# Performance work log

Hardware: AMD Instinct MI355X
Metric: run time of the kernel (lower is better)

The kernel has to match this reference:

```python
import jax, jax.numpy as jnp
import numpy as np

N, E, D, H, C, G, L = 50000, 1250000, 128, 64, 10, 128, 2


def setup_inputs() -> dict:
    key = jax.random.key(0)
    ks = jax.random.split(key, 18)
    s = lambda fan_in: 1.0 / np.sqrt(fan_in)
    inp = {
        "x": jax.random.normal(ks[0], (N, D), dtype=jnp.float32),
        "edge_index": jax.random.randint(ks[1], (2, E), 0, N, dtype=jnp.int64),
        "batch": jnp.sort(jax.random.randint(ks[2], (N,), 0, G, dtype=jnp.int64)),
        # node embedding MLP (D->H->H)
        "emb_w1": jax.random.uniform(ks[3], (D, H), jnp.float32, -s(D), s(D)),
        "emb_b1": jnp.zeros((H,), jnp.float32),
        "emb_w2": jax.random.uniform(ks[4], (H, H), jnp.float32, -s(H), s(H)),
        "emb_b2": jnp.zeros((H,), jnp.float32),
        # per-conv-block params, stacked over L layers
        "rel_w": jax.random.uniform(ks[5], (L, H, H), jnp.float32, -s(H), s(H)),
        "rel_b": jnp.zeros((L, H), jnp.float32),
        "root_w": jax.random.uniform(ks[6], (L, H, H), jnp.float32, -s(H), s(H)),
        "post_w1": jax.random.uniform(ks[7], (L, H, H), jnp.float32, -s(H), s(H)),
        "post_b1": jnp.zeros((L, H), jnp.float32),
        "post_w2": jax.random.uniform(ks[8], (L, H, H), jnp.float32, -s(H), s(H)),
        "post_b2": jnp.zeros((L, H), jnp.float32),
        # classifier
        "cls_w": jax.random.uniform(ks[9], (H, C), jnp.float32, -s(H), s(H)),
        "cls_b": jnp.zeros((C,), jnp.float32),
    }
    return inp


def _mlp(h, w1, b1, w2, b2):
    # Linear -> relu -> (dropout: identity in eval) -> Linear
    return jax.nn.relu(h @ w1 + b1) @ w2 + b2


def reference(x, edge_index, batch, emb_w1, emb_b1, emb_w2, emb_b2,
              rel_w, rel_b, root_w, post_w1, post_b1, post_w2, post_b2,
              cls_w, cls_b):
    src, dst = edge_index[0], edge_index[1]
    h = _mlp(x, emb_w1, emb_b1, emb_w2, emb_b2)  # [N,H]
    deg = jax.ops.segment_sum(jnp.ones((E,), h.dtype), dst, num_segments=N)
    inv_deg = 1.0 / jnp.maximum(deg, 1.0)  # mean aggregation, isolated nodes -> 0
    for l in range(L):
        agg = jax.ops.segment_sum(h[src], dst, num_segments=N) * inv_deg[:, None]
        h = agg @ rel_w[l] + rel_b[l] + h @ root_w[l]  # GraphConv (lin_root bias-free)
        h = _mlp(h, post_w1[l], post_b1[l], post_w2[l], post_b2[l])
        h = jax.nn.relu(h)  # dropout is identity in eval
    cnt = jax.ops.segment_sum(jnp.ones((N,), h.dtype), batch, num_segments=G)
    pooled = jax.ops.segment_sum(h, batch, num_segments=G) / jnp.maximum(cnt, 1.0)[:, None]
    return pooled @ cls_w + cls_b  # [G,C]
```

## Files before the change

kernel.cpp:

```cpp
#include <hip/hip_runtime.h>

typedef unsigned int u32;
typedef unsigned short u16;

#define NN 50000
#define EE 1250000
#define DD 128
#define HH 64
#define NCLS 10
#define NG 128
#define MAXDEG 80

#define NTILES ((NN + 63) / 64)

#define PBUK 392
#define SBLK 256
#define CHUNK ((EE + SBLK - 1) / SBLK)
#define NDP  (PBUK * 128)
#define EPKB ((CHUNK * 4 + 15) & ~15)

#define WT_LO  (8 * 4096)
#define WT_E1  (16 * 4096)
#define WT_E1L (WT_E1 + 8192)
#define WT_E2  (WT_E1 + 16384)
#define WT_E2L (WT_E2 + 4096)
#define WT_TOT (WT_E2 + 8192)


__device__ __forceinline__ u32 f2bf(float f) {
    u32 u = __float_as_uint(f);
    return (u + 0x7FFFu + ((u >> 16) & 1u)) >> 16;
}
__device__ __forceinline__ float bf2f(u16 v) {
    return __uint_as_float(((u32)v) << 16);
}

typedef __attribute__((ext_vector_type(8))) short bf16x8;
typedef __attribute__((ext_vector_type(4))) float f32x4;


__global__ __launch_bounds__(256) void k_wprep(
    const float* __restrict__ rel_w, const float* __restrict__ root_w,
    const float* __restrict__ pw1, const float* __restrict__ pw2,
    const float* __restrict__ ew1, const float* __restrict__ ew2,
    u16* __restrict__ wtb) {
    __shared__ float ldsf[128 * 65];
    const int t = threadIdx.x;
    const int m = blockIdx.x;
    if (m < 8) {
        const int layer = m >> 2, which = m & 3;
        const float* srcw =
            (which == 0 ? rel_w : which == 1 ? root_w : which == 2 ? pw1 : pw2)
            + (size_t)layer * HH * HH;
        #pragma unroll
        for (int r = 0; r < 16; ++r) {
            int idx = r * 256 + t;
            int k = idx >> 6, n = idx & 63;
            ldsf[k * 65 + n] = srcw[idx];
        }
        __syncthreads();
        #pragma unroll
        for (int r = 0; r < 16; ++r) {
            int idx = r * 256 + t;
            int n = idx >> 6, k = idx & 63;
            float v = ldsf[k * 65 + n];
            u16 hi = (u16)f2bf(v);
            u16 lo = (u16)f2bf(v - bf2f(hi));
            wtb[m * 4096 + idx] = hi;
            wtb[WT_LO + m * 4096 + idx] = lo;
        }
    } else if (m == 8) {
        #pragma unroll
        for (int r = 0; r < 32; ++r) {
            int idx = r * 256 + t;
            int k = idx >> 6, n = idx & 63;
            ldsf[k * 65 + n] = ew1[idx];
        }
        __syncthreads();
        #pragma unroll
        for (int r = 0; r < 32; ++r) {
            int idx = r * 256 + t;
            int n = idx >> 7, k = idx & 127;
            float v = ldsf[k * 65 + n];
            u16 hi = (u16)f2bf(v);
            u16 lo = (u16)f2bf(v - bf2f(hi));
            wtb[WT_E1 + idx] = hi;
            wtb[WT_E1L + idx] = lo;
        }
    } else {
        #pragma unroll
        for (int r = 0; r < 16; ++r) {
            int idx = r * 256 + t;
            int k = idx >> 6, n = idx & 63;
            ldsf[k * 65 + n] = ew2[idx];
        }
        __syncthreads();
        #pragma unroll
        for (int r = 0; r < 16; ++r) {
            int idx = r * 256 + t;
            int n = idx >> 6, k = idx & 63;
            float v = ldsf[k * 65 + n];
            u16 hi = (u16)f2bf(v);
            u16 lo = (u16)f2bf(v - bf2f(hi));
            wtb[WT_E2 + idx] = hi;
            wtb[WT_E2L + idx] = lo;
        }
    }
}


__global__ __launch_bounds__(256) void k_embed_psort(
    const float* __restrict__ x,
    const float* __restrict__ b1, const float* __restrict__ b2,
    const u16* __restrict__ wtb,
    u16* __restrict__ hb,
    const int* __restrict__ ei, u32* __restrict__ bedges,
    int* __restrict__ gboff, int* __restrict__ ghist) {
    __shared__ __align__(16) char smem[EPKB + PBUK * 8 + 32];
    const int t = threadIdx.x;

    if (blockIdx.x < SBLK) {
        u32* epk   = (u32*)smem;
        int* hist  = (int*)(smem + EPKB);
        int* boffS = hist + PBUK;
        int* wsum  = boffS + PBUK;
        const int cb = blockIdx.x;
        const int base = cb * CHUNK;
        const int n = min(CHUNK, EE - base);

        for (int b = t; b < PBUK; b += 256) hist[b] = 0;
        __syncthreads();
        for (int i0 = t; i0 < n; i0 += 2048) {
            int sV[8], dV[8];
            #pragma unroll
            for (int j = 0; j < 8; ++j) {
                int i = i0 + j * 256;
                sV[j] = -1; dV[j] = -1;
                if (i < n) { sV[j] = ei[base + i]; dV[j] = ei[EE + base + i]; }
            }
            #pragma unroll
            for (int j = 0; j < 8; ++j) {
                int i = i0 + j * 256;
                if (i < n) {
                    bool ok = (unsigned)sV[j] < NN && (unsigned)dV[j] < NN;
                    u32 w = ok ? (((u32)(dV[j] >> 7) << 23) | ((u32)sV[j] << 7) | (u32)(dV[j] & 127))
                               : 0xFFFFFFFFu;
                    epk[i] = w;
                    if (ok) atomicAdd(&hist[dV[j] >> 7], 1);
                }
            }
        }
        __syncthreads();
        int v = 0, h0 = 0;
        if (t < PBUK / 2) { h0 = hist[2 * t]; v = h0 + hist[2 * t + 1]; }
        int lane = t & 63, wd = t >> 6;
        int incl = v;
        #pragma unroll
        for (int d = 1; d < 64; d <<= 1) {
            int tt = __shfl_up(incl, d);
            if (lane >= d) incl += tt;
        }
        if (lane == 63) wsum[wd] = incl;
        __syncthreads();
        int woff = 0;
        for (int w = 0; w < wd; ++w) woff += wsum[w];
        if (t < PBUK / 2) {
            int excl = woff + incl - v;
            boffS[2 * t] = excl;
// ... 57 lines not shown
            for (int tt = 0; tt < 4; ++tt) {
                const u16* ph = wtb + WT_E1 + (tt * 16 + lr) * 128 + kc * 32 + lg * 8;
                const u16* pl = wtb + WT_E1L + (tt * 16 + lr) * 128 + kc * 32 + lg * 8;
                bf16x8 wh = *(const bf16x8*)ph;
                bf16x8 wl = *(const bf16x8*)pl;
                acc[tt] = __builtin_amdgcn_mfma_f32_16x16x32_bf16(xh, wh, acc[tt], 0, 0, 0);
                acc[tt] = __builtin_amdgcn_mfma_f32_16x16x32_bf16(xl, wh, acc[tt], 0, 0, 0);
                acc[tt] = __builtin_amdgcn_mfma_f32_16x16x32_bf16(xh, wl, acc[tt], 0, 0, 0);
            }
        }
        #pragma unroll
        for (int tt = 0; tt < 4; ++tt)
            #pragma unroll
            for (int r = 0; r < 4; ++r) {
                float v = fmaxf(acc[tt][r], 0.0f);
                u16 hi = (u16)f2bf(v);
                u16 lo = (u16)f2bf(v - bf2f(hi));
                acts0[(rowb + lg * 4 + r) * 72 + tt * 16 + lr] = hi;
                acts1[(rowb + lg * 4 + r) * 72 + tt * 16 + lr] = lo;
            }
        __syncthreads();

        bf16x8 c0h = *(const bf16x8*)&acts0[(rowb + lr) * 72 + lg * 8];
        bf16x8 c1h = *(const bf16x8*)&acts0[(rowb + lr) * 72 + 32 + lg * 8];
        bf16x8 c0l = *(const bf16x8*)&acts1[(rowb + lr) * 72 + lg * 8];
        bf16x8 c1l = *(const bf16x8*)&acts1[(rowb + lr) * 72 + 32 + lg * 8];
        f32x4 acc2[4];
        #pragma unroll
        for (int tt = 0; tt < 4; ++tt) {
            float b = b2[tt * 16 + lr];
            acc2[tt] = (f32x4){b, b, b, b};
        }
        #pragma unroll
        for (int tt = 0; tt < 4; ++tt) {
            const u16* ph = wtb + WT_E2 + (tt * 16 + lr) * 64 + lg * 8;
            const u16* pl = wtb + WT_E2L + (tt * 16 + lr) * 64 + lg * 8;
            bf16x8 wh0 = *(const bf16x8*)ph;
            bf16x8 wh1 = *(const bf16x8*)(ph + 32);
            bf16x8 wl0 = *(const bf16x8*)pl;
            bf16x8 wl1 = *(const bf16x8*)(pl + 32);
            acc2[tt] = __builtin_amdgcn_mfma_f32_16x16x32_bf16(c0h, wh0, acc2[tt], 0, 0, 0);
            acc2[tt] = __builtin_amdgcn_mfma_f32_16x16x32_bf16(c1h, wh1, acc2[tt], 0, 0, 0);
            acc2[tt] = __builtin_amdgcn_mfma_f32_16x16x32_bf16(c0l, wh0, acc2[tt], 0, 0, 0);
            acc2[tt] = __builtin_amdgcn_mfma_f32_16x16x32_bf16(c1l, wh1, acc2[tt], 0, 0, 0);
            acc2[tt] = __builtin_amdgcn_mfma_f32_16x16x32_bf16(c0h, wl0, acc2[tt], 0, 0, 0);
            acc2[tt] = __builtin_amdgcn_mfma_f32_16x16x32_bf16(c1h, wl1, acc2[tt], 0, 0, 0);
        }
        #pragma unroll
        for (int tt = 0; tt < 4; ++tt)
            #pragma unroll
            for (int r = 0; r < 4; ++r) {
                int node = nb + rowb + lg * 4 + r;
                if (node < NN)
                    hb[(size_t)node * HH + tt * 16 + lr] = (u16)f2bf(acc2[tt][r]);
            }
    }
}


__global__ __launch_bounds__(256) void k_adj(const u32* __restrict__ bedges,
                                             const int* __restrict__ gboff,
                                             const int* __restrict__ ghist,
                                             u16* __restrict__ slots,
                                             int* __restrict__ deg,
                                             float* __restrict__ pooled,
                                             u16* __restrict__ hb) {
    __shared__ u16 ls[128 * MAXDEG];
    __shared__ int lc[128];
    const int b = blockIdx.x, t = threadIdx.x;
    const int lane = t & 63, wid = t >> 6;
    if (b < (NG * HH) / 256) pooled[b * 256 + t] = 0.0f;
    if (b == 0 && t < 32) ((u32*)hb)[NN * (HH / 2) + t] = 0;
    if (t < 128) lc[t] = 0;
    {
        const u32 sent = ((u32)NN << 16) | (u32)NN;
        u32* lsu = (u32*)ls;
        for (int i = t; i < 128 * MAXDEG / 2; i += 256) lsu[i] = sent;
    }
    const int sbl = wid * 64 + lane;
    const int offv = gboff[sbl * PBUK + b];
    const int cntv = ghist[sbl * PBUK + b];
    __syncthreads();
    const int q = lane >> 4, sl = lane & 15;
    for (int it = 0; it < 16; ++it) {
        const int idx = it * 4 + q;
        const int off = __shfl(offv, idx);
        const int cnt = __shfl(cntv, idx);
        const int gbase = (wid * 64 + idx) * CHUNK + off;
        for (int i = sl; i < cnt; i += 16) {
            u32 p = bedges[gbase + i];
            int o = (int)(p & 127u);
            int src = (int)(p >> 7);
            int pos = atomicAdd(&lc[o], 1);
            if (pos < MAXDEG) ls[o * MAXDEG + pos] = (u16)src;
        }
    }
    __syncthreads();
    u32* gs = (u32*)(slots + (size_t)b * 128 * MAXDEG);
    const u32* lsu = (const u32*)ls;
    for (int i = t; i < 128 * MAXDEG / 2; i += 256) gs[i] = lsu[i];
    if (t < 128) deg[b * 128 + t] = lc[t];
}


__global__ __launch_bounds__(256) void k_agg(
    const u16* __restrict__ hb, const int* __restrict__ deg,
    const u16* __restrict__ slots, u16* __restrict__ aggb) {
    const int wid = threadIdx.x >> 6, lane = threadIdx.x & 63;
    const int half = lane >> 5, fl = lane & 31;
    const int n0 = blockIdx.x * 8 + wid * 2;
    if (n0 >= NN) return;
    const int n = n0 + half;
    const bool valid = n < NN;
    const int d = valid ? deg[n] : 0;
    const int m = min(d, MAXDEG);
    const int mp = (m + 15) & ~15;
    const u32* row = (const u32*)(slots + (size_t)n * MAXDEG);
    float s0 = 0.0f, s1 = 0.0f;
    for (int e = 0; e < mp; e += 16) {
        const u32* rp = row + (e >> 1);
        uint4 i0 = *(const uint4*)rp;
        uint4 i1 = *(const uint4*)(rp + 4);
        u32 v0 = *(const u32*)(hb + (size_t)(i0.x & 0xffffu) * HH + 2 * fl);
        u32 v1 = *(const u32*)(hb + (size_t)(i0.x >> 16)    * HH + 2 * fl);
        u32 v2 = *(const u32*)(hb + (size_t)(i0.y & 0xffffu) * HH + 2 * fl);
        u32 v3 = *(const u32*)(hb + (size_t)(i0.y >> 16)    * HH + 2 * fl);
        u32 v4 = *(const u32*)(hb + (size_t)(i0.z & 0xffffu) * HH + 2 * fl);
        u32 v5 = *(const u32*)(hb + (size_t)(i0.z >> 16)    * HH + 2 * fl);
        u32 v6 = *(const u32*)(hb + (size_t)(i0.w & 0xffffu) * HH + 2 * fl);
        u32 v7 = *(const u32*)(hb + (size_t)(i0.w >> 16)    * HH + 2 * fl);
        u32 v8 = *(const u32*)(hb + (size_t)(i1.x & 0xffffu) * HH + 2 * fl);
        u32 v9 = *(const u32*)(hb + (size_t)(i1.x >> 16)    * HH + 2 * fl);
        u32 va = *(const u32*)(hb + (size_t)(i1.y & 0xffffu) * HH + 2 * fl);
        u32 vb = *(const u32*)(hb + (size_t)(i1.y >> 16)    * HH + 2 * fl);
        u32 vc = *(const u32*)(hb + (size_t)(i1.z & 0xffffu) * HH + 2 * fl);
        u32 vd = *(const u32*)(hb + (size_t)(i1.z >> 16)    * HH + 2 * fl);
        u32 ve = *(const u32*)(hb + (size_t)(i1.w & 0xffffu) * HH + 2 * fl);
        u32 vf = *(const u32*)(hb + (size_t)(i1.w >> 16)    * HH + 2 * fl);
        s0 += ((bf2f((u16)(v0 & 0xffffu)) + bf2f((u16)(v1 & 0xffffu)))
             + (bf2f((u16)(v2 & 0xffffu)) + bf2f((u16)(v3 & 0xffffu))))
            + ((bf2f((u16)(v4 & 0xffffu)) + bf2f((u16)(v5 & 0xffffu)))
             + (bf2f((u16)(v6 & 0xffffu)) + bf2f((u16)(v7 & 0xffffu))));
        s0 += ((bf2f((u16)(v8 & 0xffffu)) + bf2f((u16)(v9 & 0xffffu)))
             + (bf2f((u16)(va & 0xffffu)) + bf2f((u16)(vb & 0xffffu))))
            + ((bf2f((u16)(vc & 0xffffu)) + bf2f((u16)(vd & 0xffffu)))
             + (bf2f((u16)(ve & 0xffffu)) + bf2f((u16)(vf & 0xffffu))));
        s1 += ((bf2f((u16)(v0 >> 16)) + bf2f((u16)(v1 >> 16)))
             + (bf2f((u16)(v2 >> 16)) + bf2f((u16)(v3 >> 16))))
            + ((bf2f((u16)(v4 >> 16)) + bf2f((u16)(v5 >> 16)))
             + (bf2f((u16)(v6 >> 16)) + bf2f((u16)(v7 >> 16))));
        s1 += ((bf2f((u16)(v8 >> 16)) + bf2f((u16)(v9 >> 16)))
             + (bf2f((u16)(va >> 16)) + bf2f((u16)(vb >> 16))))
            + ((bf2f((u16)(vc >> 16)) + bf2f((u16)(vd >> 16)))
             + (bf2f((u16)(ve >> 16)) + bf2f((u16)(vf >> 16))));
    }
    if (valid) {
        float inv = 1.0f / (float)max(d, 1);
        u32 p = f2bf(s0 * inv) | (f2bf(s1 * inv) << 16);
        ((u32*)aggb)[(size_t)n * (HH / 2) + fl] = p;
    }
}


__global__ __launch_bounds__(256) void k_dense(
    u16* __restrict__ hb, const u16* __restrict__ aggb,
    const u16* __restrict__ wt,
    const float* __restrict__ relb,
    const float* __restrict__ pb1, const float* __restrict__ pb2,
    const int* __restrict__ batch, float* __restrict__ pooled, int do_pool) {
    __shared__ __align__(16) u16 acts[2][64][72];
    const int t = threadIdx.x;
    const int w = t >> 6;
    const int l = t & 63;
    const int lr = l & 15, lg = l >> 4;
    const int rowb = w * 16;
    const int nb = blockIdx.x * 64;
    int nodeA = nb + rowb + lr;
    if (nodeA >= NN) nodeA = NN - 1;

    const u16* w_rel = wt;
    const u16* w_root = wt + 4096;
    const u16* w_p1  = wt + 2 * 4096;
    const u16* w_p2  = wt + 3 * 4096;

    const u16* agp = aggb + (size_t)nodeA * HH + lg * 8;
    const u16* hbp = hb   + (size_t)nodeA * HH + lg * 8;
    bf16x8 a0 = *(const bf16x8*)agp;
    bf16x8 a1 = *(const bf16x8*)(agp + 32);
    bf16x8 h0 = *(const bf16x8*)hbp;
    bf16x8 h1 = *(const bf16x8*)(hbp + 32);

    f32x4 acc[4];
    #pragma unroll
    for (int tt = 0; tt < 4; ++tt) {
        float b = relb[tt * 16 + lr];
        acc[tt] = (f32x4){b, b, b, b};
    }
    #pragma unroll
    for (int tt = 0; tt < 4; ++tt) {
        const u16* pr = w_rel  + (tt * 16 + lr) * 64 + lg * 8;
        const u16* po = w_root + (tt * 16 + lr) * 64 + lg * 8;
        acc[tt] = __builtin_amdgcn_mfma_f32_16x16x32_bf16(a0, *(const bf16x8*)pr,                acc[tt], 0, 0, 0);
        acc[tt] = __builtin_amdgcn_mfma_f32_16x16x32_bf16(a1, *(const bf16x8*)(pr + 32),         acc[tt], 0, 0, 0);
        acc[tt] = __builtin_amdgcn_mfma_f32_16x16x32_bf16(a0, *(const bf16x8*)(pr + WT_LO),      acc[tt], 0, 0, 0);
        acc[tt] = __builtin_amdgcn_mfma_f32_16x16x32_bf16(a1, *(const bf16x8*)(pr + WT_LO + 32), acc[tt], 0, 0, 0);
        acc[tt] = __builtin_amdgcn_mfma_f32_16x16x32_bf16(h0, *(const bf16x8*)po,                acc[tt], 0, 0, 0);
        acc[tt] = __builtin_amdgcn_mfma_f32_16x16x32_bf16(h1, *(const bf16x8*)(po + 32),         acc[tt], 0, 0, 0);
        acc[tt] = __builtin_amdgcn_mfma_f32_16x16x32_bf16(h0, *(const bf16x8*)(po + WT_LO),      acc[tt], 0, 0, 0);
        acc[tt] = __builtin_amdgcn_mfma_f32_16x16x32_bf16(h1, *(const bf16x8*)(po + WT_LO + 32), acc[tt], 0, 0, 0);
    }
    #pragma unroll
    for (int tt = 0; tt < 4; ++tt)
        #pragma unroll
        for (int r = 0; r < 4; ++r)
            acts[0][rowb + lg * 4 + r][tt * 16 + lr] = (u16)f2bf(acc[tt][r]);
    __syncthreads();

    bf16x8 c0 = *(const bf16x8*)&acts[0][rowb + lr][lg * 8];
    bf16x8 c1 = *(const bf16x8*)&acts[0][rowb + lr][32 + lg * 8];
    f32x4 acc2[4];
    #pragma unroll
    for (int tt = 0; tt < 4; ++tt) {
        float b = pb1[tt * 16 + lr];
        acc2[tt] = (f32x4){b, b, b, b};
    }
    #pragma unroll
    for (int tt = 0; tt < 4; ++tt) {
        const u16* pr = w_p1 + (tt * 16 + lr) * 64 + lg * 8;
        acc2[tt] = __builtin_amdgcn_mfma_f32_16x16x32_bf16(c0, *(const bf16x8*)pr,                acc2[tt], 0, 0, 0);
        acc2[tt] = __builtin_amdgcn_mfma_f32_16x16x32_bf16(c1, *(const bf16x8*)(pr + 32),         acc2[tt], 0, 0, 0);
        acc2[tt] = __builtin_amdgcn_mfma_f32_16x16x32_bf16(c0, *(const bf16x8*)(pr + WT_LO),      acc2[tt], 0, 0, 0);
        acc2[tt] = __builtin_amdgcn_mfma_f32_16x16x32_bf16(c1, *(const bf16x8*)(pr + WT_LO + 32), acc2[tt], 0, 0, 0);
    }
    #pragma unroll
    for (int tt = 0; tt < 4; ++tt)
        #pragma unroll
        for (int r = 0; r < 4; ++r)
            acts[1][rowb + lg * 4 + r][tt * 16 + lr] = (u16)f2bf(fmaxf(acc2[tt][r], 0.0f));
    __syncthreads();

    bf16x8 d0 = *(const bf16x8*)&acts[1][rowb + lr][lg * 8];
    bf16x8 d1 = *(const bf16x8*)&acts[1][rowb + lr][32 + lg * 8];
    f32x4 acc3[4];
    #pragma unroll
    for (int tt = 0; tt < 4; ++tt) {
        float b = pb2[tt * 16 + lr];
        acc3[tt] = (f32x4){b, b, b, b};
    }
    #pragma unroll
    for (int tt = 0; tt < 4; ++tt) {
        const u16* pr = w_p2 + (tt * 16 + lr) * 64 + lg * 8;
        acc3[tt] = __builtin_amdgcn_mfma_f32_16x16x32_bf16(d0, *(const bf16x8*)pr,                acc3[tt], 0, 0, 0);
        acc3[tt] = __builtin_amdgcn_mfma_f32_16x16x32_bf16(d1, *(const bf16x8*)(pr + 32),         acc3[tt], 0, 0, 0);
        acc3[tt] = __builtin_amdgcn_mfma_f32_16x16x32_bf16(d0, *(const bf16x8*)(pr + WT_LO),      acc3[tt], 0, 0, 0);
        acc3[tt] = __builtin_amdgcn_mfma_f32_16x16x32_bf16(d1, *(const bf16x8*)(pr + WT_LO + 32), acc3[tt], 0, 0, 0);
    }

    if (!do_pool) {
        #pragma unroll
        for (int tt = 0; tt < 4; ++tt)
            #pragma unroll
            for (int r = 0; r < 4; ++r) {
                int node = nb + rowb + lg * 4 + r;
                if (node < NN)
                    hb[(size_t)node * HH + tt * 16 + lr] = (u16)f2bf(fmaxf(acc3[tt][r], 0.0f));
            }
    } else {
        #pragma unroll
        for (int tt = 0; tt < 4; ++tt)
            #pragma unroll
            for (int r = 0; r < 4; ++r)
                acts[0][rowb + lg * 4 + r][tt * 16 + lr] = (u16)f2bf(fmaxf(acc3[tt][r], 0.0f));
        __syncthreads();
        if (t < HH) {
            const int f = t;
            const int n1 = min(64, NN - nb);
            int cur = batch[nb];
            float s = 0.0f;
            for (int i = 0; i < n1; ++i) {
                int g = batch[nb + i];
                if (g != cur) {
                    if ((unsigned)cur < NG) atomicAdd(&pooled[cur * HH + f], s);
                    s = 0.0f; cur = g;
                }
                s += bf2f(acts[0][i][f]);
            }
            if ((unsigned)cur < NG) atomicAdd(&pooled[cur * HH + f], s);
        }
    }
}


__global__ void k_cls(const float* __restrict__ pooled, const int* __restrict__ batch,
                      const float* __restrict__ w, const float* __restrict__ b,
                      float* __restrict__ out) {
    const int g = blockIdx.x;
    const int t = threadIdx.x;
    if (t >= NCLS) return;
    int lo = 0, hi = NN;
    while (lo < hi) { int mid = (lo + hi) >> 1; if (batch[mid] < g) lo = mid + 1; else hi = mid; }
    const int beg = lo;
    lo = 0; hi = NN;
    while (lo < hi) { int mid = (lo + hi) >> 1; if (batch[mid] < g + 1) lo = mid + 1; else hi = mid; }
    const int cnt = lo - beg;
    const float inv = 1.0f / (float)max(cnt, 1);
    float o = b[t];
    #pragma unroll 8
    for (int k = 0; k < HH; ++k) o += pooled[g * HH + k] * inv * w[k * NCLS + t];
    out[g * NCLS + t] = o;
}


extern "C" void kernel_launch(void* const* d_in, const int* in_sizes, int n_in,
                              void* d_out, int out_size, void* d_ws, size_t ws_size,
                              hipStream_t stream) {
    const float* x      = (const float*)d_in[0];
    const int*   ei     = (const int*)d_in[1];
    const int*   batch  = (const int*)d_in[2];
    const float* emb_w1 = (const float*)d_in[3];
    const float* emb_b1 = (const float*)d_in[4];
    const float* emb_w2 = (const float*)d_in[5];
    const float* emb_b2 = (const float*)d_in[6];
    const float* rel_w  = (const float*)d_in[7];
    const float* rel_b  = (const float*)d_in[8];
    const float* root_w = (const float*)d_in[9];
    const float* pw1    = (const float*)d_in[10];
    const float* pb1    = (const float*)d_in[11];
    const float* pw2    = (const float*)d_in[12];
    const float* pb2    = (const float*)d_in[13];
    const float* cls_w  = (const float*)d_in[14];
    const float* cls_b  = (const float*)d_in[15];
    float* out = (float*)d_out;

    char* ws = (char*)d_ws;
    size_t off = 0;
    auto alloc = [&](size_t bytes) -> void* {
        off = (off + 255) & ~(size_t)255;
        void* p = ws + off;
        off += bytes;
        return p;
    };
    u16*   hb     = (u16*)alloc((size_t)(NN + 1) * HH * 2);
    u16*   aggb   = (u16*)alloc((size_t)NN * HH * 2);
    u32*   bedges = (u32*)aggb;
    u16*   slots  = (u16*)alloc((size_t)NDP * MAXDEG * 2);
    int*   deg    = (int*)alloc((size_t)NDP * 4);
    int*   gboff  = (int*)alloc((size_t)SBLK * PBUK * 4);
    int*   ghist  = (int*)alloc((size_t)SBLK * PBUK * 4);
    float* pooled = (float*)alloc((size_t)NG * HH * 4);
    u16*   wtb    = (u16*)alloc((size_t)WT_TOT * 2);

    k_wprep<<<10, 256, 0, stream>>>(rel_w, root_w, pw1, pw2, emb_w1, emb_w2, wtb);
    k_embed_psort<<<SBLK + NTILES, 256, 0, stream>>>(
        x, emb_b1, emb_b2, wtb, hb, ei, bedges, gboff, ghist);
    k_adj<<<PBUK, 256, 0, stream>>>(bedges, gboff, ghist, slots, deg, pooled, hb);
    k_agg<<<(NN + 7) / 8, 256, 0, stream>>>(hb, deg, slots, aggb);
    k_dense<<<NTILES, 256, 0, stream>>>(hb, aggb, wtb, rel_b, pb1, pb2, batch, pooled, 0);
    k_agg<<<(NN + 7) / 8, 256, 0, stream>>>(hb, deg, slots, aggb);
    k_dense<<<NTILES, 256, 0, stream>>>(hb, aggb, wtb + 4 * 4096,
                                        rel_b + HH, pb1 + HH, pb2 + HH,
                                        batch, pooled, 1);
    k_cls<<<NG, 64, 0, stream>>>(pooled, batch, cls_w, cls_b, out);
}
```

Before: 262.0 us.

## Fuse neighbor aggregation into dense kernel and fold classifier into last block

```diff
diff --git a/kernel.cpp b/kernel.cpp
--- a/kernel.cpp
+++ b/kernel.cpp
@@ -289,13 +289,19 @@
                                              u16* __restrict__ slots,
                                              int* __restrict__ deg,
                                              float* __restrict__ pooled,
-                                             u16* __restrict__ hb) {
+                                             u16* __restrict__ hbA,
+                                             u16* __restrict__ hbB,
+                                             int* __restrict__ ctr) {
     __shared__ u16 ls[128 * MAXDEG];
     __shared__ int lc[128];
     const int b = blockIdx.x, t = threadIdx.x;
     const int lane = t & 63, wid = t >> 6;
     if (b < (NG * HH) / 256) pooled[b * 256 + t] = 0.0f;
-    if (b == 0 && t < 32) ((u32*)hb)[NN * (HH / 2) + t] = 0;
+    if (b == 0) {
+        if (t < 32) ((u32*)hbA)[NN * (HH / 2) + t] = 0;
+        else if (t < 64) ((u32*)hbB)[NN * (HH / 2) + (t - 32)] = 0;
+        else if (t == 64) *ctr = 0;
+    }
     if (t < 128) lc[t] = 0;
     {
         const u32 sent = ((u32)NN << 16) | (u32)NN;
@@ -328,90 +334,94 @@
 }
 
 
-__global__ __launch_bounds__(256) void k_agg(
-    const u16* __restrict__ hb, const int* __restrict__ deg,
-    const u16* __restrict__ slots, u16* __restrict__ aggb) {
-    const int wid = threadIdx.x >> 6, lane = threadIdx.x & 63;
-    const int half = lane >> 5, fl = lane & 31;
-    const int n0 = blockIdx.x * 8 + wid * 2;
-    if (n0 >= NN) return;
-    const int n = n0 + half;
-    const bool valid = n < NN;
-    const int d = valid ? deg[n] : 0;
-    const int m = min(d, MAXDEG);
-    const int mp = (m + 15) & ~15;
-    const u32* row = (const u32*)(slots + (size_t)n * MAXDEG);
-    float s0 = 0.0f, s1 = 0.0f;
-    for (int e = 0; e < mp; e += 16) {
-        const u32* rp = row + (e >> 1);
-        uint4 i0 = *(const uint4*)rp;
-        uint4 i1 = *(const uint4*)(rp + 4);
-        u32 v0 = *(const u32*)(hb + (size_t)(i0.x & 0xffffu) * HH + 2 * fl);
-        u32 v1 = *(const u32*)(hb + (size_t)(i0.x >> 16)    * HH + 2 * fl);
-        u32 v2 = *(const u32*)(hb + (size_t)(i0.y & 0xffffu) * HH + 2 * fl);
-        u32 v3 = *(const u32*)(hb + (size_t)(i0.y >> 16)    * HH + 2 * fl);
-        u32 v4 = *(const u32*)(hb + (size_t)(i0.z & 0xffffu) * HH + 2 * fl);
-        u32 v5 = *(const u32*)(hb + (size_t)(i0.z >> 16)    * HH + 2 * fl);
-        u32 v6 = *(const u32*)(hb + (size_t)(i0.w & 0xffffu) * HH + 2 * fl);
-        u32 v7 = *(const u32*)(hb + (size_t)(i0.w >> 16)    * HH + 2 * fl);
-        u32 v8 = *(const u32*)(hb + (size_t)(i1.x & 0xffffu) * HH + 2 * fl);
-        u32 v9 = *(const u32*)(hb + (size_t)(i1.x >> 16)    * HH + 2 * fl);
-        u32 va = *(const u32*)(hb + (size_t)(i1.y & 0xffffu) * HH + 2 * fl);
-        u32 vb = *(const u32*)(hb + (size_t)(i1.y >> 16)    * HH + 2 * fl);
-        u32 vc = *(const u32*)(hb + (size_t)(i1.z & 0xffffu) * HH + 2 * fl);
-        u32 vd = *(const u32*)(hb + (size_t)(i1.z >> 16)    * HH + 2 * fl);
-        u32 ve = *(const u32*)(hb + (size_t)(i1.w & 0xffffu) * HH + 2 * fl);
-        u32 vf = *(const u32*)(hb + (size_t)(i1.w >> 16)    * HH + 2 * fl);
-        s0 += ((bf2f((u16)(v0 & 0xffffu)) + bf2f((u16)(v1 & 0xffffu)))
-             + (bf2f((u16)(v2 & 0xffffu)) + bf2f((u16)(v3 & 0xffffu))))
-            + ((bf2f((u16)(v4 & 0xffffu)) + bf2f((u16)(v5 & 0xffffu)))
-             + (bf2f((u16)(v6 & 0xffffu)) + bf2f((u16)(v7 & 0xffffu))));
-        s0 += ((bf2f((u16)(v8 & 0xffffu)) + bf2f((u16)(v9 & 0xffffu)))
-             + (bf2f((u16)(va & 0xffffu)) + bf2f((u16)(vb & 0xffffu))))
-            + ((bf2f((u16)(vc & 0xffffu)) + bf2f((u16)(vd & 0xffffu)))
-             + (bf2f((u16)(ve & 0xffffu)) + bf2f((u16)(vf & 0xffffu))));
-        s1 += ((bf2f((u16)(v0 >> 16)) + bf2f((u16)(v1 >> 16)))
-             + (bf2f((u16)(v2 >> 16)) + bf2f((u16)(v3 >> 16))))
-            + ((bf2f((u16)(v4 >> 16)) + bf2f((u16)(v5 >> 16)))
-             + (bf2f((u16)(v6 >> 16)) + bf2f((u16)(v7 >> 16))));
-        s1 += ((bf2f((u16)(v8 >> 16)) + bf2f((u16)(v9 >> 16)))
-             + (bf2f((u16)(va >> 16)) + bf2f((u16)(vb >> 16))))
-            + ((bf2f((u16)(vc >> 16)) + bf2f((u16)(vd >> 16)))
-             + (bf2f((u16)(ve >> 16)) + bf2f((u16)(vf >> 16))));
-    }
-    if (valid) {
-        float inv = 1.0f / (float)max(d, 1);
-        u32 p = f2bf(s0 * inv) | (f2bf(s1 * inv) << 16);
-        ((u32*)aggb)[(size_t)n * (HH / 2) + fl] = p;
-    }
-}
-
-
 __global__ __launch_bounds__(256) void k_dense(
-    u16* __restrict__ hb, const u16* __restrict__ aggb,
+    const u16* __restrict__ hsrc,
+    u16* __restrict__ hdst,
+    const int* __restrict__ deg, const u16* __restrict__ slots,
     const u16* __restrict__ wt,
     const float* __restrict__ relb,
     const float* __restrict__ pb1, const float* __restrict__ pb2,
-    const int* __restrict__ batch, float* __restrict__ pooled, int do_pool) {
-    __shared__ __align__(16) u16 acts[2][64][72];
+    const int* __restrict__ batch, float* __restrict__ pooled,
+    int* __restrict__ ctr,
+    const float* __restrict__ clsw, const float* __restrict__ clsb,
+    float* __restrict__ outp, int do_pool) {
+    __shared__ __align__(16) char smemd[NG * HH * 4];
+    u16 (*acts)[64][72] = (u16 (*)[64][72])smemd;
     const int t = threadIdx.x;
     const int w = t >> 6;
-    const int l = t & 63;
-    const int lr = l & 15, lg = l >> 4;
+    const int lane = t & 63;
+    const int lr = lane & 15, lg = lane >> 4;
     const int rowb = w * 16;
     const int nb = blockIdx.x * 64;
+
+    {
+        const int half = lane >> 5, fl = lane & 31;
+        const int degv = deg[nb + rowb + (lane & 15)];
+        for (int p = 0; p < 8; ++p) {
+            const int row = rowb + 2 * p + half;
+            const int node = nb + row;
+            const bool valid = node < NN;
+            const int d = __shfl(degv, 2 * p + half);
+            const int m = min(valid ? d : 0, MAXDEG);
+            const int mp = (m + 15) & ~15;
+            const u32* rowp = (const u32*)(slots + (size_t)node * MAXDEG);
+            float s0 = 0.0f, s1 = 0.0f;
+            for (int e = 0; e < mp; e += 16) {
+                const u32* rp = rowp + (e >> 1);
+                uint4 i0 = *(const uint4*)rp;
+                uint4 i1 = *(const uint4*)(rp + 4);
+                u32 v0 = *(const u32*)(hsrc + (size_t)(i0.x & 0xffffu) * HH + 2 * fl);
+                u32 v1 = *(const u32*)(hsrc + (size_t)(i0.x >> 16)    * HH + 2 * fl);
+                u32 v2 = *(const u32*)(hsrc + (size_t)(i0.y & 0xffffu) * HH + 2 * fl);
+                u32 v3 = *(const u32*)(hsrc + (size_t)(i0.y >> 16)    * HH + 2 * fl);
+                u32 v4 = *(const u32*)(hsrc + (size_t)(i0.z & 0xffffu) * HH + 2 * fl);
+                u32 v5 = *(const u32*)(hsrc + (size_t)(i0.z >> 16)    * HH + 2 * fl);
+                u32 v6 = *(const u32*)(hsrc + (size_t)(i0.w & 0xffffu) * HH + 2 * fl);
+                u32 v7 = *(const u32*)(hsrc + (size_t)(i0.w >> 16)    * HH + 2 * fl);
+                u32 v8 = *(const u32*)(hsrc + (size_t)(i1.x & 0xffffu) * HH + 2 * fl);
+                u32 v9 = *(const u32*)(hsrc + (size_t)(i1.x >> 16)    * HH + 2 * fl);
+                u32 va = *(const u32*)(hsrc + (size_t)(i1.y & 0xffffu) * HH + 2 * fl);
+                u32 vb = *(const u32*)(hsrc + (size_t)(i1.y >> 16)    * HH + 2 * fl);
+                u32 vc = *(const u32*)(hsrc + (size_t)(i1.z & 0xffffu) * HH + 2 * fl);
+                u32 vd = *(const u32*)(hsrc + (size_t)(i1.z >> 16)    * HH + 2 * fl);
+                u32 ve = *(const u32*)(hsrc + (size_t)(i1.w & 0xffffu) * HH + 2 * fl);
+                u32 vf = *(const u32*)(hsrc + (size_t)(i1.w >> 16)    * HH + 2 * fl);
+                s0 += ((bf2f((u16)(v0 & 0xffffu)) + bf2f((u16)(v1 & 0xffffu)))
+                     + (bf2f((u16)(v2 & 0xffffu)) + bf2f((u16)(v3 & 0xffffu))))
+                    + ((bf2f((u16)(v4 & 0xffffu)) + bf2f((u16)(v5 & 0xffffu)))
+                     + (bf2f((u16)(v6 & 0xffffu)) + bf2f((u16)(v7 & 0xffffu))));
+                s0 += ((bf2f((u16)(v8 & 0xffffu)) + bf2f((u16)(v9 & 0xffffu)))
+                     + (bf2f((u16)(va & 0xffffu)) + bf2f((u16)(vb & 0xffffu))))
+                    + ((bf2f((u16)(vc & 0xffffu)) + bf2f((u16)(vd & 0xffffu)))
+                     + (bf2f((u16)(ve & 0xffffu)) + bf2f((u16)(vf & 0xffffu))));
+                s1 += ((bf2f((u16)(v0 >> 16)) + bf2f((u16)(v1 >> 16)))
+                     + (bf2f((u16)(v2 >> 16)) + bf2f((u16)(v3 >> 16))))
+                    + ((bf2f((u16)(v4 >> 16)) + bf2f((u16)(v5 >> 16)))
+                     + (bf2f((u16)(v6 >> 16)) + bf2f((u16)(v7 >> 16))));
+                s1 += ((bf2f((u16)(v8 >> 16)) + bf2f((u16)(v9 >> 16)))
+                     + (bf2f((u16)(va >> 16)) + bf2f((u16)(vb >> 16))))
+                    + ((bf2f((u16)(vc >> 16)) + bf2f((u16)(vd >> 16)))
+                     + (bf2f((u16)(ve >> 16)) + bf2f((u16)(vf >> 16))));
+            }
+            if (valid) {
+                float inv = 1.0f / (float)max(d, 1);
+                u32 pk = f2bf(s0 * inv) | (f2bf(s1 * inv) << 16);
+                ((u32*)&acts[0][row][0])[fl] = pk;
+            }
+        }
+    }
+    __syncthreads();
+
     int nodeA = nb + rowb + lr;
     if (nodeA >= NN) nodeA = NN - 1;
-
     const u16* w_rel = wt;
     const u16* w_root = wt + 4096;
     const u16* w_p1  = wt + 2 * 4096;
     const u16* w_p2  = wt + 3 * 4096;
 
-    const u16* agp = aggb + (size_t)nodeA * HH + lg * 8;
-    const u16* hbp = hb   + (size_t)nodeA * HH + lg * 8;
-    bf16x8 a0 = *(const bf16x8*)agp;
-    bf16x8 a1 = *(const bf16x8*)(agp + 32);
+    const u16* hbp = hsrc + (size_t)nodeA * HH + lg * 8;
+    bf16x8 a0 = *(const bf16x8*)&acts[0][rowb + lr][lg * 8];
+    bf16x8 a1 = *(const bf16x8*)&acts[0][rowb + lr][32 + lg * 8];
     bf16x8 h0 = *(const bf16x8*)hbp;
     bf16x8 h1 = *(const bf16x8*)(hbp + 32);
 
@@ -438,11 +448,11 @@
     for (int tt = 0; tt < 4; ++tt)
         #pragma unroll
         for (int r = 0; r < 4; ++r)
-            acts[0][rowb + lg * 4 + r][tt * 16 + lr] = (u16)f2bf(acc[tt][r]);
-    __syncthreads();
-
-    bf16x8 c0 = *(const bf16x8*)&acts[0][rowb + lr][lg * 8];
-    bf16x8 c1 = *(const bf16x8*)&acts[0][rowb + lr][32 + lg * 8];
+            acts[1][rowb + lg * 4 + r][tt * 16 + lr] = (u16)f2bf(acc[tt][r]);
+    __syncthreads();
+
+    bf16x8 c0 = *(const bf16x8*)&acts[1][rowb + lr][lg * 8];
+    bf16x8 c1 = *(const bf16x8*)&acts[1][rowb + lr][32 + lg * 8];
     f32x4 acc2[4];
     #pragma unroll
     for (int tt = 0; tt < 4; ++tt) {
@@ -457,15 +467,16 @@
         acc2[tt] = __builtin_amdgcn_mfma_f32_16x16x32_bf16(c0, *(const bf16x8*)(pr + WT_LO),      acc2[tt], 0, 0, 0);
         acc2[tt] = __builtin_amdgcn_mfma_f32_16x16x32_bf16(c1, *(const bf16x8*)(pr + WT_LO + 32), acc2[tt], 0, 0, 0);
     }
+    __syncthreads();
     #pragma unroll
     for (int tt = 0; tt < 4; ++tt)
         #pragma unroll
         for (int r = 0; r < 4; ++r)
-            acts[1][rowb + lg * 4 + r][tt * 16 + lr] = (u16)f2bf(fmaxf(acc2[tt][r], 0.0f));
-    __syncthreads();
-
-    bf16x8 d0 = *(const bf16x8*)&acts[1][rowb + lr][lg * 8];
-    bf16x8 d1 = *(const bf16x8*)&acts[1][rowb + lr][32 + lg * 8];
+            acts[0][rowb + lg * 4 + r][tt * 16 + lr] = (u16)f2bf(fmaxf(acc2[tt][r], 0.0f));
+    __syncthreads();
+
+    bf16x8 d0 = *(const bf16x8*)&acts[0][rowb + lr][lg * 8];
+    bf16x8 d1 = *(const bf16x8*)&acts[0][rowb + lr][32 + lg * 8];
     f32x4 acc3[4];
     #pragma unroll
     for (int tt = 0; tt < 4; ++tt) {
@@ -488,51 +499,66 @@
             for (int r = 0; r < 4; ++r) {
                 int node = nb + rowb + lg * 4 + r;
                 if (node < NN)
-                    hb[(size_t)node * HH + tt * 16 + lr] = (u16)f2bf(fmaxf(acc3[tt][r], 0.0f));
-            }
-    } else {
-        #pragma unroll
-        for (int tt = 0; tt < 4; ++tt)
-            #pragma unroll
-            for (int r = 0; r < 4; ++r)
-                acts[0][rowb + lg * 4 + r][tt * 16 + lr] = (u16)f2bf(fmaxf(acc3[tt][r], 0.0f));
-        __syncthreads();
-        if (t < HH) {
-            const int f = t;
-            const int n1 = min(64, NN - nb);
-            int cur = batch[nb];
-            float s = 0.0f;
-            for (int i = 0; i < n1; ++i) {
-                int g = batch[nb + i];
-                if (g != cur) {
-                    if ((unsigned)cur < NG) atomicAdd(&pooled[cur * HH + f], s);
-                    s = 0.0f; cur = g;
-                }
-                s += bf2f(acts[0][i][f]);
-            }
-            if ((unsigned)cur < NG) atomicAdd(&pooled[cur * HH + f], s);
-        }
-    }
-}
-
-
-__global__ void k_cls(const float* __restrict__ pooled, const int* __restrict__ batch,
-                      const float* __restrict__ w, const float* __restrict__ b,
-                      float* __restrict__ out) {
-    const int g = blockIdx.x;
-    const int t = threadIdx.x;
-    if (t >= NCLS) return;
-    int lo = 0, hi = NN;
-    while (lo < hi) { int mid = (lo + hi) >> 1; if (batch[mid] < g) lo = mid + 1; else hi = mid; }
-    const int beg = lo;
-    lo = 0; hi = NN;
-    while (lo < hi) { int mid = (lo + hi) >> 1; if (batch[mid] < g + 1) lo = mid + 1; else hi = mid; }
-    const int cnt = lo - beg;
-    const float inv = 1.0f / (float)max(cnt, 1);
-    float o = b[t];
-    #pragma unroll 8
-    for (int k = 0; k < HH; ++k) o += pooled[g * HH + k] * inv * w[k * NCLS + t];
-    out[g * NCLS + t] = o;
+                    hdst[(size_t)node * HH + tt * 16 + lr] = (u16)f2bf(fmaxf(acc3[tt][r], 0.0f));
+            }
+        return;
+    }
+
+    __syncthreads();
+    #pragma unroll
+    for (int tt = 0; tt < 4; ++tt)
+        #pragma unroll
+        for (int r = 0; r < 4; ++r)
+            acts[1][rowb + lg * 4 + r][tt * 16 + lr] = (u16)f2bf(fmaxf(acc3[tt][r], 0.0f));
+    __syncthreads();
+    if (t < HH) {
+        const int f = t;
+        const int n1 = min(64, NN - nb);
+        int cur = batch[nb];
+        float s = 0.0f;
+        for (int i = 0; i < n1; ++i) {
+            int g = batch[nb + i];
+            if (g != cur) {
+                if ((unsigned)cur < NG) atomicAdd(&pooled[cur * HH + f], s);
+                s = 0.0f; cur = g;
+            }
+            s += bf2f(acts[1][i][f]);
+        }
+        if ((unsigned)cur < NG) atomicAdd(&pooled[cur * HH + f], s);
+    }
+
+    __threadfence();
+    __shared__ int lastF;
+    if (t == 0) lastF = (atomicAdd(ctr, 1) == NTILES - 1);
+    __syncthreads();
+    if (!lastF) return;
+
+    __shared__ float ginv[NG];
+    if (t < NG) {
+        int g = t;
+        int lo = 0, hi = NN;
+        while (lo < hi) { int mid = (lo + hi) >> 1; if (batch[mid] < g) lo = mid + 1; else hi = mid; }
+        int beg = lo; lo = 0; hi = NN;
+        while (lo < hi) { int mid = (lo + hi) >> 1; if (batch[mid] < g + 1) lo = mid + 1; else hi = mid; }
+        ginv[g] = 1.0f / (float)max(lo - beg, 1);
+    }
+    float* plbuf = (float*)smemd;
+    #pragma unroll
+    for (int j = 0; j < (NG * HH) / 256; ++j) {
+        int idx = t * 32 + j;
+        int g = idx >> 6, k = idx & 63;
+        float v = atomicAdd(&pooled[idx], 0.0f);
+        plbuf[k * NG + g] = v;
+    }
+    __syncthreads();
+    for (int o = t; o < NG * NCLS; o += 256) {
+        int g = o / NCLS, c = o - g * NCLS;
+        float s = 0.0f;
+        #pragma unroll 8
+        for (int k = 0; k < HH; ++k)
+            s += plbuf[k * NG + g] * clsw[k * NCLS + c];
+        outp[o] = clsb[c] + s * ginv[g];
+    }
 }
 
 
@@ -565,25 +591,25 @@
         off += bytes;
         return p;
     };
-    u16*   hb     = (u16*)alloc((size_t)(NN + 1) * HH * 2);
-    u16*   aggb   = (u16*)alloc((size_t)NN * HH * 2);
-    u32*   bedges = (u32*)aggb;
+    u16*   hbA    = (u16*)alloc((size_t)(NN + 1) * HH * 2);
+    u16*   hbB    = (u16*)alloc((size_t)(NN + 1) * HH * 2);
+    u32*   bedges = (u32*)hbB;
     u16*   slots  = (u16*)alloc((size_t)NDP * MAXDEG * 2);
     int*   deg    = (int*)alloc((size_t)NDP * 4);
     int*   gboff  = (int*)alloc((size_t)SBLK * PBUK * 4);
     int*   ghist  = (int*)alloc((size_t)SBLK * PBUK * 4);
     float* pooled = (float*)alloc((size_t)NG * HH * 4);
+    int*   ctr    = (int*)alloc(256);
     u16*   wtb    = (u16*)alloc((size_t)WT_TOT * 2);
 
     k_wprep<<<10, 256, 0, stream>>>(rel_w, root_w, pw1, pw2, emb_w1, emb_w2, wtb);
     k_embed_psort<<<SBLK + NTILES, 256, 0, stream>>>(
-        x, emb_b1, emb_b2, wtb, hb, ei, bedges, gboff, ghist);
-    k_adj<<<PBUK, 256, 0, stream>>>(bedges, gboff, ghist, slots, deg, pooled, hb);
-    k_agg<<<(NN + 7) / 8, 256, 0, stream>>>(hb, deg, slots, aggb);
-    k_dense<<<NTILES, 256, 0, stream>>>(hb, aggb, wtb, rel_b, pb1, pb2, batch, pooled, 0);
-    k_agg<<<(NN + 7) / 8, 256, 0, stream>>>(hb, deg, slots, aggb);
-    k_dense<<<NTILES, 256, 0, stream>>>(hb, aggb, wtb + 4 * 4096,
-                                        rel_b + HH, pb1 + HH, pb2 + HH,
-                                        batch, pooled, 1);
-    k_cls<<<NG, 64, 0, stream>>>(pooled, batch, cls_w, cls_b, out);
+        x, emb_b1, emb_b2, wtb, hbA, ei, bedges, gboff, ghist);
+    k_adj<<<PBUK, 256, 0, stream>>>(bedges, gboff, ghist, slots, deg, pooled, hbA, hbB, ctr);
+    k_dense<<<NTILES, 256, 0, stream>>>(hbA, hbB, deg, slots, wtb,
+                                        rel_b, pb1, pb2, batch, pooled, ctr,
+                                        cls_w, cls_b, out, 0);
+    k_dense<<<NTILES, 256, 0, stream>>>(hbB, hbB, deg, slots, wtb + 4 * 4096,
+                                        rel_b + HH, pb1 + HH, pb2 + HH, batch, pooled, ctr,
+                                        cls_w, cls_b, out, 1);
 }
```

Result: slower. 321.0 us (+22.5%).

## Split node features into two 32-wide planes for cache-friendly gather aggregation

Applied to the files above, without the earlier changes.

```diff
diff --git a/kernel.cpp b/kernel.cpp
--- a/kernel.cpp
+++ b/kernel.cpp
@@ -10,6 +10,7 @@
 #define NCLS 10
 #define NG 128
 #define MAXDEG 80
+#define MAXD2 96
 
 #define NTILES ((NN + 63) / 64)
 
@@ -18,6 +19,8 @@
 #define CHUNK ((EE + SBLK - 1) / SBLK)
 #define NDP  (PBUK * 128)
 #define EPKB ((CHUNK * 4 + 15) & ~15)
+
+#define PLSZ ((size_t)(NN + 1) * 32)
 
 #define WT_LO  (8 * 4096)
 #define WT_E1  (16 * 4096)
@@ -37,6 +40,7 @@
 
 typedef __attribute__((ext_vector_type(8))) short bf16x8;
 typedef __attribute__((ext_vector_type(4))) float f32x4;
+typedef __attribute__((ext_vector_type(4))) u32 u32x4;
 
 
 __global__ __launch_bounds__(256) void k_wprep(
@@ -113,7 +117,7 @@
     const float* __restrict__ x,
     const float* __restrict__ b1, const float* __restrict__ b2,
     const u16* __restrict__ wtb,
-    u16* __restrict__ hb,
+    u16* __restrict__ hpl,
     const int* __restrict__ ei, u32* __restrict__ bedges,
     int* __restrict__ gboff, int* __restrict__ ghist) {
     __shared__ __align__(16) char smem[EPKB + PBUK * 8 + 32];
@@ -277,7 +281,8 @@
             for (int r = 0; r < 4; ++r) {
                 int node = nb + rowb + lg * 4 + r;
                 if (node < NN)
-                    hb[(size_t)node * HH + tt * 16 + lr] = (u16)f2bf(acc2[tt][r]);
+                    hpl[(size_t)(tt >> 1) * PLSZ + (size_t)node * 32 + (tt & 1) * 16 + lr]
+                        = (u16)f2bf(acc2[tt][r]);
             }
     }
 }
@@ -289,18 +294,21 @@
                                              u16* __restrict__ slots,
                                              int* __restrict__ deg,
                                              float* __restrict__ pooled,
-                                             u16* __restrict__ hb) {
-    __shared__ u16 ls[128 * MAXDEG];
+                                             u16* __restrict__ hpl) {
+    __shared__ u16 ls[128 * MAXD2];
     __shared__ int lc[128];
     const int b = blockIdx.x, t = threadIdx.x;
     const int lane = t & 63, wid = t >> 6;
     if (b < (NG * HH) / 256) pooled[b * 256 + t] = 0.0f;
-    if (b == 0 && t < 32) ((u32*)hb)[NN * (HH / 2) + t] = 0;
+    if (b == 0) {
+        if (t < 16) ((u32*)hpl)[(size_t)NN * 16 + t] = 0;
+        else if (t < 32) ((u32*)hpl)[PLSZ / 2 + (size_t)NN * 16 + (t - 16)] = 0;
+    }
     if (t < 128) lc[t] = 0;
     {
         const u32 sent = ((u32)NN << 16) | (u32)NN;
         u32* lsu = (u32*)ls;
-        for (int i = t; i < 128 * MAXDEG / 2; i += 256) lsu[i] = sent;
+        for (int i = t; i < 128 * MAXD2 / 2; i += 256) lsu[i] = sent;
     }
     const int sbl = wid * 64 + lane;
     const int offv = gboff[sbl * PBUK + b];
@@ -317,51 +325,59 @@
             int o = (int)(p & 127u);
             int src = (int)(p >> 7);
             int pos = atomicAdd(&lc[o], 1);
-            if (pos < MAXDEG) ls[o * MAXDEG + pos] = (u16)src;
+            if (pos < MAXDEG) ls[o * MAXD2 + pos] = (u16)src;
         }
     }
     __syncthreads();
-    u32* gs = (u32*)(slots + (size_t)b * 128 * MAXDEG);
+    u32* gs = (u32*)(slots + (size_t)b * 128 * MAXD2);
     const u32* lsu = (const u32*)ls;
-    for (int i = t; i < 128 * MAXDEG / 2; i += 256) gs[i] = lsu[i];
+    for (int i = t; i < 128 * MAXD2 / 2; i += 256) gs[i] = lsu[i];
     if (t < 128) deg[b * 128 + t] = lc[t];
 }
 
 
-__global__ __launch_bounds__(256) void k_agg(
-    const u16* __restrict__ hb, const int* __restrict__ deg,
-    const u16* __restrict__ slots, u16* __restrict__ aggb) {
-    const int wid = threadIdx.x >> 6, lane = threadIdx.x & 63;
-    const int half = lane >> 5, fl = lane & 31;
-    const int n0 = blockIdx.x * 8 + wid * 2;
-    if (n0 >= NN) return;
-    const int n = n0 + half;
-    const bool valid = n < NN;
-    const int d = valid ? deg[n] : 0;
-    const int m = min(d, MAXDEG);
-    const int mp = (m + 15) & ~15;
-    const u32* row = (const u32*)(slots + (size_t)n * MAXDEG);
+__device__ __forceinline__ void agg_pass(const u16* __restrict__ pl,
+                                         const u32* __restrict__ row,
+                                         int mp, int fl, float& r0, float& r1) {
     float s0 = 0.0f, s1 = 0.0f;
-    for (int e = 0; e < mp; e += 16) {
-        const u32* rp = row + (e >> 1);
-        uint4 i0 = *(const uint4*)rp;
-        uint4 i1 = *(const uint4*)(rp + 4);
-        u32 v0 = *(const u32*)(hb + (size_t)(i0.x & 0xffffu) * HH + 2 * fl);
-        u32 v1 = *(const u32*)(hb + (size_t)(i0.x >> 16)    * HH + 2 * fl);
-        u32 v2 = *(const u32*)(hb + (size_t)(i0.y & 0xffffu) * HH + 2 * fl);
-        u32 v3 = *(const u32*)(hb + (size_t)(i0.y >> 16)    * HH + 2 * fl);
-        u32 v4 = *(const u32*)(hb + (size_t)(i0.z & 0xffffu) * HH + 2 * fl);
-        u32 v5 = *(const u32*)(hb + (size_t)(i0.z >> 16)    * HH + 2 * fl);
-        u32 v6 = *(const u32*)(hb + (size_t)(i0.w & 0xffffu) * HH + 2 * fl);
-        u32 v7 = *(const u32*)(hb + (size_t)(i0.w >> 16)    * HH + 2 * fl);
-        u32 v8 = *(const u32*)(hb + (size_t)(i1.x & 0xffffu) * HH + 2 * fl);
-        u32 v9 = *(const u32*)(hb + (size_t)(i1.x >> 16)    * HH + 2 * fl);
-        u32 va = *(const u32*)(hb + (size_t)(i1.y & 0xffffu) * HH + 2 * fl);
-        u32 vb = *(const u32*)(hb + (size_t)(i1.y >> 16)    * HH + 2 * fl);
-        u32 vc = *(const u32*)(hb + (size_t)(i1.z & 0xffffu) * HH + 2 * fl);
-        u32 vd = *(const u32*)(hb + (size_t)(i1.z >> 16)    * HH + 2 * fl);
-        u32 ve = *(const u32*)(hb + (size_t)(i1.w & 0xffffu) * HH + 2 * fl);
-        u32 vf = *(const u32*)(hb + (size_t)(i1.w >> 16)    * HH + 2 * fl);
+    for (int e = 0; e < mp; e += 32) {
+        const u32x4* rp = (const u32x4*)(row + (e >> 1));
+        u32x4 i0 = __builtin_nontemporal_load(rp);
+        u32x4 i1 = __builtin_nontemporal_load(rp + 1);
+        u32x4 i2 = __builtin_nontemporal_load(rp + 2);
+        u32x4 i3 = __builtin_nontemporal_load(rp + 3);
+        u32 v0 = *(const u32*)(pl + (size_t)(i0[0] & 0xffffu) * 32 + 2 * fl);
+        u32 v1 = *(const u32*)(pl + (size_t)(i0[0] >> 16)     * 32 + 2 * fl);
+        u32 v2 = *(const u32*)(pl + (size_t)(i0[1] & 0xffffu) * 32 + 2 * fl);
+        u32 v3 = *(const u32*)(pl + (size_t)(i0[1] >> 16)     * 32 + 2 * fl);
+        u32 v4 = *(const u32*)(pl + (size_t)(i0[2] & 0xffffu) * 32 + 2 * fl);
+        u32 v5 = *(const u32*)(pl + (size_t)(i0[2] >> 16)     * 32 + 2 * fl);
+        u32 v6 = *(const u32*)(pl + (size_t)(i0[3] & 0xffffu) * 32 + 2 * fl);
+        u32 v7 = *(const u32*)(pl + (size_t)(i0[3] >> 16)     * 32 + 2 * fl);
+        u32 v8 = *(const u32*)(pl + (size_t)(i1[0] & 0xffffu) * 32 + 2 * fl);
+        u32 v9 = *(const u32*)(pl + (size_t)(i1[0] >> 16)     * 32 + 2 * fl);
+        u32 va = *(const u32*)(pl + (size_t)(i1[1] & 0xffffu) * 32 + 2 * fl);
+        u32 vb = *(const u32*)(pl + (size_t)(i1[1] >> 16)     * 32 + 2 * fl);
+        u32 vc = *(const u32*)(pl + (size_t)(i1[2] & 0xffffu) * 32 + 2 * fl);
+        u32 vd = *(const u32*)(pl + (size_t)(i1[2] >> 16)     * 32 + 2 * fl);
+        u32 ve = *(const u32*)(pl + (size_t)(i1[3] & 0xffffu) * 32 + 2 * fl);
+        u32 vf = *(const u32*)(pl + (size_t)(i1[3] >> 16)     * 32 + 2 * fl);
+        u32 w0 = *(const u32*)(pl + (size_t)(i2[0] & 0xffffu) * 32 + 2 * fl);
+        u32 w1 = *(const u32*)(pl + (size_t)(i2[0] >> 16)     * 32 + 2 * fl);
+        u32 w2 = *(const u32*)(pl + (size_t)(i2[1] & 0xffffu) * 32 + 2 * fl);
+        u32 w3 = *(const u32*)(pl + (size_t)(i2[1] >> 16)     * 32 + 2 * fl);
+        u32 w4 = *(const u32*)(pl + (size_t)(i2[2] & 0xffffu) * 32 + 2 * fl);
+        u32 w5 = *(const u32*)(pl + (size_t)(i2[2] >> 16)     * 32 + 2 * fl);
+        u32 w6 = *(const u32*)(pl + (size_t)(i2[3] & 0xffffu) * 32 + 2 * fl);
+        u32 w7 = *(const u32*)(pl + (size_t)(i2[3] >> 16)     * 32 + 2 * fl);
+        u32 w8 = *(const u32*)(pl + (size_t)(i3[0] & 0xffffu) * 32 + 2 * fl);
+        u32 w9 = *(const u32*)(pl + (size_t)(i3[0] >> 16)     * 32 + 2 * fl);
+        u32 wa = *(const u32*)(pl + (size_t)(i3[1] & 0xffffu) * 32 + 2 * fl);
+        u32 wb = *(const u32*)(pl + (size_t)(i3[1] >> 16)     * 32 + 2 * fl);
+        u32 wc = *(const u32*)(pl + (size_t)(i3[2] & 0xffffu) * 32 + 2 * fl);
+        u32 wd = *(const u32*)(pl + (size_t)(i3[2] >> 16)     * 32 + 2 * fl);
+        u32 we = *(const u32*)(pl + (size_t)(i3[3] & 0xffffu) * 32 + 2 * fl);
+        u32 wf = *(const u32*)(pl + (size_t)(i3[3] >> 16)     * 32 + 2 * fl);
         s0 += ((bf2f((u16)(v0 & 0xffffu)) + bf2f((u16)(v1 & 0xffffu)))
              + (bf2f((u16)(v2 & 0xffffu)) + bf2f((u16)(v3 & 0xffffu))))
             + ((bf2f((u16)(v4 & 0xffffu)) + bf2f((u16)(v5 & 0xffffu)))
@@ -370,6 +386,14 @@
              + (bf2f((u16)(va & 0xffffu)) + bf2f((u16)(vb & 0xffffu))))
             + ((bf2f((u16)(vc & 0xffffu)) + bf2f((u16)(vd & 0xffffu)))
              + (bf2f((u16)(ve & 0xffffu)) + bf2f((u16)(vf & 0xffffu))));
+        s0 += ((bf2f((u16)(w0 & 0xffffu)) + bf2f((u16)(w1 & 0xffffu)))
+             + (bf2f((u16)(w2 & 0xffffu)) + bf2f((u16)(w3 & 0xffffu))))
+            + ((bf2f((u16)(w4 & 0xffffu)) + bf2f((u16)(w5 & 0xffffu)))
+             + (bf2f((u16)(w6 & 0xffffu)) + bf2f((u16)(w7 & 0xffffu))));
+        s0 += ((bf2f((u16)(w8 & 0xffffu)) + bf2f((u16)(w9 & 0xffffu)))
+             + (bf2f((u16)(wa & 0xffffu)) + bf2f((u16)(wb & 0xffffu))))
+            + ((bf2f((u16)(wc & 0xffffu)) + bf2f((u16)(wd & 0xffffu)))
+             + (bf2f((u16)(we & 0xffffu)) + bf2f((u16)(wf & 0xffffu))));
         s1 += ((bf2f((u16)(v0 >> 16)) + bf2f((u16)(v1 >> 16)))
              + (bf2f((u16)(v2 >> 16)) + bf2f((u16)(v3 >> 16))))
             + ((bf2f((u16)(v4 >> 16)) + bf2f((u16)(v5 >> 16)))
@@ -378,17 +402,40 @@
              + (bf2f((u16)(va >> 16)) + bf2f((u16)(vb >> 16))))
             + ((bf2f((u16)(vc >> 16)) + bf2f((u16)(vd >> 16)))
              + (bf2f((u16)(ve >> 16)) + bf2f((u16)(vf >> 16))));
-    }
-    if (valid) {
-        float inv = 1.0f / (float)max(d, 1);
-        u32 p = f2bf(s0 * inv) | (f2bf(s1 * inv) << 16);
-        ((u32*)aggb)[(size_t)n * (HH / 2) + fl] = p;
-    }
+        s1 += ((bf2f((u16)(w0 >> 16)) + bf2f((u16)(w1 >> 16)))
+             + (bf2f((u16)(w2 >> 16)) + bf2f((u16)(w3 >> 16))))
+            + ((bf2f((u16)(w4 >> 16)) + bf2f((u16)(w5 >> 16)))
+             + (bf2f((u16)(w6 >> 16)) + bf2f((u16)(w7 >> 16))));
+        s1 += ((bf2f((u16)(w8 >> 16)) + bf2f((u16)(w9 >> 16)))
+             + (bf2f((u16)(wa >> 16)) + bf2f((u16)(wb >> 16))))
+            + ((bf2f((u16)(wc >> 16)) + bf2f((u16)(wd >> 16)))
+             + (bf2f((u16)(we >> 16)) + bf2f((u16)(wf >> 16))));
+    }
+    r0 = s0; r1 = s1;
+}
+
+__global__ __launch_bounds__(256) void k_agg(
+    const u16* __restrict__ hpl, const int* __restrict__ deg,
+    const u16* __restrict__ slots, u16* __restrict__ aggb) {
+    const int wid = threadIdx.x >> 6, lane = threadIdx.x & 63;
+    const int ng = lane >> 4, fl = lane & 15;
+    const int n = blockIdx.x * 16 + wid * 4 + ng;
+    const int d = deg[n];
+    const int m = min(d, MAXDEG);
+    const int mp = (m + 31) & ~31;
+    const u32* row = (const u32*)(slots + (size_t)n * MAXD2);
+    float sA0, sA1, sB0, sB1;
+    agg_pass(hpl, row, mp, fl, sA0, sA1);
+    agg_pass(hpl + PLSZ, row, mp, fl, sB0, sB1);
+    float inv = 1.0f / (float)max(d, 1);
+    u32* ob = (u32*)aggb + (size_t)n * (HH / 2);
+    __builtin_nontemporal_store(f2bf(sA0 * inv) | (f2bf(sA1 * inv) << 16), ob + fl);
+    __builtin_nontemporal_store(f2bf(sB0 * inv) | (f2bf(sB1 * inv) << 16), ob + 16 + fl);
 }
 
 
 __global__ __launch_bounds__(256) void k_dense(
-    u16* __restrict__ hb, const u16* __restrict__ aggb,
+    u16* __restrict__ hpl, const u16* __restrict__ aggb,
     const u16* __restrict__ wt,
     const float* __restrict__ relb,
     const float* __restrict__ pb1, const float* __restrict__ pb2,
@@ -409,11 +456,11 @@
     const u16* w_p2  = wt + 3 * 4096;
 
     const u16* agp = aggb + (size_t)nodeA * HH + lg * 8;
-    const u16* hbp = hb   + (size_t)nodeA * HH + lg * 8;
+    const u16* hp0 = hpl + (size_t)nodeA * 32 + lg * 8;
     bf16x8 a0 = *(const bf16x8*)agp;
     bf16x8 a1 = *(const bf16x8*)(agp + 32);
-    bf16x8 h0 = *(const bf16x8*)hbp;
-    bf16x8 h1 = *(const bf16x8*)(hbp + 32);
+    bf16x8 h0 = *(const bf16x8*)hp0;
+    bf16x8 h1 = *(const bf16x8*)(hp0 + PLSZ);
 
     f32x4 acc[4];
     #pragma unroll
@@ -488,7 +535,8 @@
             for (int r = 0; r < 4; ++r) {
                 int node = nb + rowb + lg * 4 + r;
                 if (node < NN)
-                    hb[(size_t)node * HH + tt * 16 + lr] = (u16)f2bf(fmaxf(acc3[tt][r], 0.0f));
+                    hpl[(size_t)(tt >> 1) * PLSZ + (size_t)node * 32 + (tt & 1) * 16 + lr]
+                        = (u16)f2bf(fmaxf(acc3[tt][r], 0.0f));
             }
     } else {
         #pragma unroll
@@ -565,10 +613,10 @@
         off += bytes;
         return p;
     };
-    u16*   hb     = (u16*)alloc((size_t)(NN + 1) * HH * 2);
+    u16*   hpl    = (u16*)alloc(2 * PLSZ * 2);
     u16*   aggb   = (u16*)alloc((size_t)NN * HH * 2);
     u32*   bedges = (u32*)aggb;
-    u16*   slots  = (u16*)alloc((size_t)NDP * MAXDEG * 2);
+    u16*   slots  = (u16*)alloc((size_t)NDP * MAXD2 * 2);
     int*   deg    = (int*)alloc((size_t)NDP * 4);
     int*   gboff  = (int*)alloc((size_t)SBLK * PBUK * 4);
     int*   ghist  = (int*)alloc((size_t)SBLK * PBUK * 4);
@@ -577,12 +625,12 @@
 
     k_wprep<<<10, 256, 0, stream>>>(rel_w, root_w, pw1, pw2, emb_w1, emb_w2, wtb);
     k_embed_psort<<<SBLK + NTILES, 256, 0, stream>>>(
-        x, emb_b1, emb_b2, wtb, hb, ei, bedges, gboff, ghist);
-    k_adj<<<PBUK, 256, 0, stream>>>(bedges, gboff, ghist, slots, deg, pooled, hb);
-    k_agg<<<(NN + 7) / 8, 256, 0, stream>>>(hb, deg, slots, aggb);
-    k_dense<<<NTILES, 256, 0, stream>>>(hb, aggb, wtb, rel_b, pb1, pb2, batch, pooled, 0);
-    k_agg<<<(NN + 7) / 8, 256, 0, stream>>>(hb, deg, slots, aggb);
-    k_dense<<<NTILES, 256, 0, stream>>>(hb, aggb, wtb + 4 * 4096,
+        x, emb_b1, emb_b2, wtb, hpl, ei, bedges, gboff, ghist);
+    k_adj<<<PBUK, 256, 0, stream>>>(bedges, gboff, ghist, slots, deg, pooled, hpl);
+    k_agg<<<NN / 16, 256, 0, stream>>>(hpl, deg, slots, aggb);
+    k_dense<<<NTILES, 256, 0, stream>>>(hpl, aggb, wtb, rel_b, pb1, pb2, batch, pooled, 0);
+    k_agg<<<NN / 16, 256, 0, stream>>>(hpl, deg, slots, aggb);
+    k_dense<<<NTILES, 256, 0, stream>>>(hpl, aggb, wtb + 4 * 4096,
                                         rel_b + HH, pb1 + HH, pb2 + HH,
                                         batch, pooled, 1);
     k_cls<<<NG, 64, 0, stream>>>(pooled, batch, cls_w, cls_b, out);
```

Measured after the change: 280.9 us. 1.07x slower.
